# Performance work log

Measured on AMD Instinct MI355X. Metric: run time of the kernel, lower is better.

## Reference

```python
import jax, jax.numpy as jnp
import numpy as np

B, N, E, F, C = 4, 10000, 160000, 128, 128
NUM_ITERATIONS = 3  # num_iterations init arg


def setup_inputs() -> dict:
    key = jax.random.key(0)
    ks = jax.random.split(key, 8)
    objects = jax.random.normal(ks[0], (B, N, F), dtype=jnp.float32)
    connections = jax.random.randint(ks[1], (B, E, 2), 0, N, dtype=jnp.int32)
    # small init scales keep exp() in the attention numerically tame (mirrors
    # glorot/orthogonal-scale weights at init)
    object_state_W = jax.random.normal(ks[2], (F, C), dtype=jnp.float32) * (1.0 / np.sqrt(F))
    state_attention_W = jax.random.normal(ks[3], (C, C), dtype=jnp.float32) * 0.05
    linked_state_attention_W = jax.random.normal(ks[4], (C, C), dtype=jnp.float32) * 0.05
    linked_state_W = jax.random.normal(ks[5], (C, C), dtype=jnp.float32) * (1.0 / np.sqrt(C))
    attention_b = jnp.zeros((C,), dtype=jnp.float32)
    state_b = jnp.zeros((C,), dtype=jnp.float32)
    return {
        "objects": objects,
        "object_state_W": object_state_W,
        "state_attention_W": state_attention_W,
        "linked_state_attention_W": linked_state_attention_W,
        "attention_b": attention_b,
        "linked_state_W": linked_state_W,
        "state_b": state_b,
        "connections": connections,
    }


def reference(objects, object_state_W, state_attention_W, linked_state_attention_W,
              attention_b, linked_state_W, state_b, connections):
    # bidirectional: double edges with both orientations  [B, 2E]
    src = jnp.concatenate([connections[:, :, 0], connections[:, :, 1]], axis=1)
    dst = jnp.concatenate([connections[:, :, 1], connections[:, :, 0]], axis=1)

    # initial states: [B, N, C]
    states = jnp.tanh(jnp.einsum('bnf,fc->bnc', objects, object_state_W) + state_b)

    def step_one(states_b, src_b, dst_b):
        # states_b: [N, C]; src_b/dst_b: [2E]
        states_aW = states_b @ state_attention_W          # [N, C]
        linked_aW = states_b @ linked_state_attention_W   # [N, C]
        # per-edge unnormalized attention  [2E, C]
        attention = jnp.exp(states_aW[src_b] + linked_aW[dst_b] + attention_b)
        # scatter-add normalization; self edge contributes 1 (exp(0))
        attention_norm = jnp.ones_like(states_b).at[src_b].add(attention)  # [N, C]
        self_attention = 1.0 / attention_norm
        attention = attention / attention_norm[src_b]
        # weighted neighbor aggregation
        attented = attention * states_b[dst_b]                              # [2E, C]
        linked_gated = jnp.zeros_like(states_b).at[src_b].add(attented)     # [N, C]
        return jnp.tanh(states_b * self_attention + linked_gated @ linked_state_W + state_b)

    step = jax.vmap(step_one)
    for _ in range(NUM_ITERATIONS):
        states = step(states, src, dst)
    return states
```

## Files before the change

kernel.cpp:

```cpp
#include <hip/hip_runtime.h>
#include <hip/hip_bf16.h>


#define BATCH 4
#define NNODE 10000
#define NEDGE 160000
#define TWOE  (2*NEDGE)
#define MROWS (BATCH*NNODE)
#define NCHUNK 64
#define CHUNKE (NEDGE/NCHUNK)
#define PADN  10240

typedef unsigned short u16;
typedef unsigned int   u32;
typedef __attribute__((ext_vector_type(8))) short bf16x8_t;
typedef __attribute__((ext_vector_type(4))) float f32x4_t;

__device__ __forceinline__ float b2f(u16 h){ return __uint_as_float(((u32)h) << 16); }
__device__ __forceinline__ u16 f2bf(float f){
  u32 u = __float_as_uint(f);
  return (u16)((u + 0x7fffu + ((u >> 16) & 1u)) >> 16);
}
__device__ __forceinline__ float fast_tanh(float x){
  float e = __expf(2.0f * x);
  return fmaf(-2.0f, __builtin_amdgcn_rcpf(e + 1.0f), 1.0f);
}

__global__ void detect_dtype(const u32* __restrict__ objw, int* __restrict__ flag){
  __shared__ int zc, hc;
  if (threadIdx.x == 0){ zc = 0; hc = 0; }
  __syncthreads();
  int z = 0, h = 0;
  for (int i = threadIdx.x; i < 1024; i += 256){
    u32 lo = objw[i] & 0xffffu;
    if (lo == 0) z++;
    if (((lo >> 7) & 0xffu) >= 160u) h++;
  }
  atomicAdd(&zc, z); atomicAdd(&hc, h);
  __syncthreads();
  if (threadIdx.x == 0) *flag = (hc > 0 || zc > 512) ? 1 : 0;
}

__global__ void prep_weights(const void* __restrict__ Wo, const void* __restrict__ Wa,
                             const void* __restrict__ Wla, const void* __restrict__ Wl,
                             const void* __restrict__ ab, const void* __restrict__ sb,
                             const int* __restrict__ flag, u16* __restrict__ Wt,
                             float* __restrict__ biasf){
  int idx = blockIdx.x * 256 + threadIdx.x;
  bool f = (*flag != 0);
  if (idx < 65536){
    int m = idx >> 14, k = (idx >> 7) & 127, c = idx & 127;
    const void* src = (m == 0) ? Wo : (m == 1) ? Wa : (m == 2) ? Wla : Wl;
    u16 h = f ? f2bf(((const float*)src)[k * 128 + c]) : ((const u16*)src)[k * 128 + c];
    Wt[m * 16384 + c * 128 + k] = h;
  } else {
    int t = idx - 65536;
    const void* src = (t < 128) ? sb : ab;
    int i = t & 127;
    biasf[t] = f ? ((const float*)src)[i] : b2f(((const u16*)src)[i]);
  }
}

__device__ __forceinline__ void chunk_of(int blk, int& b, int& c){
  int xcd = blk & 7;
  b = xcd >> 1;
  c = ((blk >> 3) << 1) | (xcd & 1);
}

__global__ void __launch_bounds__(256) csr_hist(const int* __restrict__ conn,
                                                u16* __restrict__ partial){
  int b, c; chunk_of(blockIdx.x, b, c);
  __shared__ u32 hist[NNODE];
  for (int n = threadIdx.x; n < NNODE; n += 256) hist[n] = 0;
  __syncthreads();
  const int2* cp = (const int2*)conn + (size_t)b * NEDGE + c * CHUNKE;
  for (int i = threadIdx.x; i < CHUNKE; i += 256){
    int2 e = cp[i];
    atomicAdd(&hist[e.x], 1);
    atomicAdd(&hist[e.y], 1);
  }
  __syncthreads();
  u16* prow = partial + (size_t)(b * NCHUNK + c) * PADN;
  for (int n = threadIdx.x; n < NNODE; n += 256) prow[n] = (u16)hist[n];
}

__global__ void __launch_bounds__(256) csr_colscan(u16* __restrict__ partial,
    int* __restrict__ row_start, int* __restrict__ bsum){
  int b = blockIdx.x / 40, w = blockIdx.x % 40;
  int n = w * 256 + threadIdx.x;
  u32 run = 0;
  if (n < NNODE){
    #pragma unroll 8
    for (int c = 0; c < NCHUNK; c++){
      size_t idx = (size_t)(b * NCHUNK + c) * PADN + n;
      u32 v = partial[idx];
      partial[idx] = (u16)run;
      run += v;
    }
  }
  __shared__ u32 buf[256];
  buf[threadIdx.x] = run;
  __syncthreads();
  for (int off = 1; off < 256; off <<= 1){
    u32 x = (threadIdx.x >= (unsigned)off) ? buf[threadIdx.x - off] : 0;
    __syncthreads();
    buf[threadIdx.x] += x;
    __syncthreads();
  }
  u32 incl = buf[threadIdx.x];
  if (n < NNODE) row_start[b * (NNODE + 1) + n] = (int)(incl - run);
  if (threadIdx.x == 255) bsum[blockIdx.x] = (int)incl;
}

__global__ void scanB(const int* __restrict__ bsum, int* __restrict__ boff,
                      int* __restrict__ row_start){
  __shared__ int s[160];
  if (threadIdx.x < 160) s[threadIdx.x] = bsum[threadIdx.x];
  __syncthreads();
  if (threadIdx.x < 160){
    int b = threadIdx.x / 40, j = threadIdx.x % 40;
    int off = 0;
    for (int q = b * 40; q < b * 40 + j; q++) off += s[q];
    boff[threadIdx.x] = off;
  }
  if (threadIdx.x < BATCH) row_start[threadIdx.x * (NNODE + 1) + NNODE] = TWOE;
}

__global__ void scanC(int* __restrict__ row_start, const int* __restrict__ boff){
  int b = blockIdx.x / 40, j = blockIdx.x % 40;
  int n = j * 256 + threadIdx.x;
  if (n < NNODE) row_start[b * (NNODE + 1) + n] += boff[blockIdx.x];
}

__global__ void __launch_bounds__(256) csr_fill(const int* __restrict__ conn,
    const u16* __restrict__ partial, const int* __restrict__ row_start,
    int* __restrict__ edge_dst){
  int b, c; chunk_of(blockIdx.x, b, c);
  __shared__ u32 cur[NNODE];
  const u16* prow = partial + (size_t)(b * NCHUNK + c) * PADN;
  const int* rs = row_start + b * (NNODE + 1);
  for (int n = threadIdx.x; n < NNODE; n += 256) cur[n] = (u32)rs[n] + prow[n];
  __syncthreads();
  const int2* cp = (const int2*)conn + (size_t)b * NEDGE + c * CHUNKE;
  int* edb = edge_dst + (size_t)b * TWOE;
  for (int i = threadIdx.x; i < CHUNKE; i += 256){
    int2 e = cp[i];
    u32 p1 = atomicAdd(&cur[e.x], 1); edb[p1] = e.y;
    u32 p2 = atomicAdd(&cur[e.y], 1); edb[p2] = e.x;
  }
}

__device__ __forceinline__ void gemm_tile4(const u16* __restrict__ arow,
    const u16* __restrict__ wt, int lm, int lq, int cofs, f32x4_t acc[4]){
  #pragma unroll
  for (int ks = 0; ks < 4; ks++){
    bf16x8_t a = *(const bf16x8_t*)(arow + ks * 32);
    #pragma unroll
    for (int nb = 0; nb < 4; nb++){
      bf16x8_t bfr = *(const bf16x8_t*)(wt + (cofs + nb * 16 + lm) * 128 + ks * 32 + lq * 8);
      acc[nb] = __builtin_amdgcn_mfma_f32_16x16x32_bf16(a, bfr, acc[nb], 0, 0, 0);
    }
  }
}

__device__ __forceinline__ void gemm_tile4_packed(const u32* __restrict__ Lrow,
    const u16* __restrict__ wt, int lm, int lq, int cofs, f32x4_t acc[4]){
  #pragma unroll
  for (int ks = 0; ks < 4; ks++){
    uint4 wa = *(const uint4*)(Lrow + ks * 32 + lq * 8);
    uint4 wb = *(const uint4*)(Lrow + ks * 32 + lq * 8 + 4);
    bf16x8_t a;
    a[0] = (short)wa.x; a[1] = (short)wa.y; a[2] = (short)wa.z; a[3] = (short)wa.w;
    a[4] = (short)wb.x; a[5] = (short)wb.y; a[6] = (short)wb.z; a[7] = (short)wb.w;
    #pragma unroll
    for (int nb = 0; nb < 4; nb++){
      bf16x8_t bfr = *(const bf16x8_t*)(wt + (cofs + nb * 16 + lm) * 128 + ks * 32 + lq * 8);
      acc[nb] = __builtin_amdgcn_mfma_f32_16x16x32_bf16(a, bfr, acc[nb], 0, 0, 0);
    }
  }
}

__device__ __forceinline__ void phase2_awlaw4(const u16* __restrict__ ldstile,
    const u16* __restrict__ Wt, const float* __restrict__ biasf,
    int lm, int lq, int cofs, int r0, float* __restrict__ awsa,
    u32* __restrict__ ghw){
  const u16* Wta  = Wt + 16384;
  const u16* Wtla = Wt + 32768;
  const u16* ldsrow = ldstile + lm * 136 + lq * 8;
  f32x4_t accA[4], accL[4];
  #pragma unroll
  for (int i = 0; i < 4; i++){ accA[i] = (f32x4_t){0.f,0.f,0.f,0.f}; accL[i] = (f32x4_t){0.f,0.f,0.f,0.f}; }
  #pragma unroll
  for (int ks = 0; ks < 4; ks++){
    bf16x8_t a = *(const bf16x8_t*)(ldsrow + ks * 32);
    #pragma unroll
    for (int nb = 0; nb < 4; nb++){
      bf16x8_t ba = *(const bf16x8_t*)(Wta  + (cofs + nb * 16 + lm) * 128 + ks * 32 + lq * 8);
      bf16x8_t bl = *(const bf16x8_t*)(Wtla + (cofs + nb * 16 + lm) * 128 + ks * 32 + lq * 8);
      accA[nb] = __builtin_amdgcn_mfma_f32_16x16x32_bf16(a, ba, accA[nb], 0, 0, 0);
      accL[nb] = __builtin_amdgcn_mfma_f32_16x16x32_bf16(a, bl, accL[nb], 0, 0, 0);
    }
  }
  #pragma unroll
  for (int nb = 0; nb < 4; nb++){
    int col = cofs + nb * 16 + lm;
    float bb = biasf[128 + col];
    #pragma unroll
    for (int i = 0; i < 4; i++){
      int row = r0 + lq * 4 + i;
      awsa[(size_t)row * 128 + col] = accA[nb][i];
      u16 el = f2bf(__expf(accL[nb][i] + bb));
      u16 s  = ldstile[(lq * 4 + i) * 136 + col];
      ghw[(size_t)row * 64 + (col & 63)] = (u32)el | ((u32)s << 16);
    }
  }
}

__global__ void __launch_bounds__(256) fused_init(const void* __restrict__ obj_raw,
    const int* __restrict__ flag, const u16* __restrict__ Wt,
    const float* __restrict__ biasf, float* __restrict__ awsa,
    u32* __restrict__ gat0, u32* __restrict__ gat1){
  __shared__ u16 lds[2][16 * 136];
  const int lane = threadIdx.x & 63, wave = threadIdx.x >> 6;
  const int t = wave >> 1, ch = wave & 1, cofs = ch * 64;
  const int r0 = blockIdx.x * 32 + t * 16;
  const int lm = lane & 15, lq = lane >> 4;
  f32x4_t acc[4];
  #pragma unroll
  for (int i = 0; i < 4; i++) acc[i] = (f32x4_t){0.f, 0.f, 0.f, 0.f};
  if (*flag){
    const float* arow = (const float*)obj_raw + (size_t)(r0 + lm) * 128 + lq * 8;
    #pragma unroll
    for (int ks = 0; ks < 4; ks++){
      float4 fa = *(const float4*)(arow + ks * 32);
      float4 fb = *(const float4*)(arow + ks * 32 + 4);
      bf16x8_t a;
      a[0] = (short)f2bf(fa.x); a[1] = (short)f2bf(fa.y);
      a[2] = (short)f2bf(fa.z); a[3] = (short)f2bf(fa.w);
      a[4] = (short)f2bf(fb.x); a[5] = (short)f2bf(fb.y);
      a[6] = (short)f2bf(fb.z); a[7] = (short)f2bf(fb.w);
      #pragma unroll
      for (int nb = 0; nb < 4; nb++){
        bf16x8_t bfr = *(const bf16x8_t*)(Wt + (cofs + nb * 16 + lm) * 128 + ks * 32 + lq * 8);
        acc[nb] = __builtin_amdgcn_mfma_f32_16x16x32_bf16(a, bfr, acc[nb], 0, 0, 0);
      }
    }
  } else {
    gemm_tile4((const u16*)obj_raw + (size_t)(r0 + lm) * 128 + lq * 8, Wt, lm, lq, cofs, acc);
  }
  #pragma unroll
  for (int nb = 0; nb < 4; nb++){
    int col = cofs + nb * 16 + lm;
    float bb = biasf[col];
    #pragma unroll
    for (int i = 0; i < 4; i++)
      lds[t][(lq * 4 + i) * 136 + col] = f2bf(fast_tanh(acc[nb][i] + bb));
  }
  __syncthreads();
  phase2_awlaw4(&lds[t][0], Wt, biasf, lm, lq, cofs, r0, awsa, ch ? gat1 : gat0);
}

__global__ void __launch_bounds__(256) fused_mid(const u32* __restrict__ lgsa,
    const u16* __restrict__ Wt, const float* __restrict__ biasf,
    float* __restrict__ awsa, u32* __restrict__ gat0, u32* __restrict__ gat1){
  __shared__ u16 lds[2][16 * 136];
  const int lane = threadIdx.x & 63, wave = threadIdx.x >> 6;
  const int t = wave >> 1, ch = wave & 1, cofs = ch * 64;
  const int r0 = blockIdx.x * 32 + t * 16;
  const int lm = lane & 15, lq = lane >> 4;
  f32x4_t acc[4];
  #pragma unroll
  for (int i = 0; i < 4; i++) acc[i] = (f32x4_t){0.f, 0.f, 0.f, 0.f};
  gemm_tile4_packed(lgsa + (size_t)(r0 + lm) * 128, Wt + 49152, lm, lq, cofs, acc);
  #pragma unroll
  for (int nb = 0; nb < 4; nb++){
    int col = cofs + nb * 16 + lm;
    float bb = biasf[col];
    #pragma unroll
    for (int i = 0; i < 4; i++){
      int row = r0 + lq * 4 + i;
      u32 v = lgsa[(size_t)row * 128 + col];
      u16 hb = (u16)(v >> 16);
      float sa = (float)(*(const _Float16*)&hb);
      lds[t][(lq * 4 + i) * 136 + col] = f2bf(fast_tanh(sa + acc[nb][i] + bb));
    }
  }
  __syncthreads();
  phase2_awlaw4(&lds[t][0], Wt, biasf, lm, lq, cofs, r0, awsa, ch ? gat1 : gat0);
}

__global__ void __launch_bounds__(256) final_out(const u32* __restrict__ lgsa,
    const u16* __restrict__ Wt, const float* __restrict__ biasf,
    const int* __restrict__ flag, void* __restrict__ outp){
  const int lane = threadIdx.x & 63, wave = threadIdx.x >> 6;
  const int t = wave >> 1, ch = wave & 1, cofs = ch * 64;
  const int r0 = blockIdx.x * 32 + t * 16;
  const int lm = lane & 15, lq = lane >> 4;
  bool f32out = (*flag != 0);
  f32x4_t acc[4];
  #pragma unroll
  for (int i = 0; i < 4; i++) acc[i] = (f32x4_t){0.f, 0.f, 0.f, 0.f};
  gemm_tile4_packed(lgsa + (size_t)(r0 + lm) * 128, Wt + 49152, lm, lq, cofs, acc);
  #pragma unroll
  for (int nb = 0; nb < 4; nb++){
    int col = cofs + nb * 16 + lm;
    float bb = biasf[col];
    #pragma unroll
    for (int i = 0; i < 4; i++){
      int row = r0 + lq * 4 + i;
      u32 vv = lgsa[(size_t)row * 128 + col];
      u16 hb = (u16)(vv >> 16);
      float sa = (float)(*(const _Float16*)&hb);
      float v = fast_tanh(sa + acc[nb][i] + bb);
      if (f32out) ((float*)outp)[(size_t)row * 128 + col] = v;
      else        ((u16*)  outp)[(size_t)row * 128 + col] = f2bf(v);
    }
  }
}

__device__ __forceinline__ void acc_e(u32 g, float& s1, float& s2){
  float el = __uint_as_float(g << 16);
  float sv = __uint_as_float(g & 0xffff0000u);
  s1 += el;
  s2 = fmaf(el, sv, s2);
}

__global__ void __launch_bounds__(256) edge_kernel(const float* __restrict__ awsa,
    const u32* __restrict__ gat0, const u32* __restrict__ gat1,
    const int* __restrict__ row_start, const int* __restrict__ edge_dst,
    u32* __restrict__ lgsa){
  int blk = blockIdx.x;
  int xcd = blk & 7;
  int b = xcd >> 1, h = xcd & 1;
  int i = blk >> 3;
  int n = i * 4 + (int)(threadIdx.x >> 6);
  int node = b * NNODE + n;
  int c = threadIdx.x & 63;
  const u32* gh = (h ? gat1 : gat0) + (size_t)b * NNODE * 64;
  int e0 = __builtin_amdgcn_readfirstlane(row_start[b * (NNODE + 1) + n]);
  int e1 = __builtin_amdgcn_readfirstlane(row_start[b * (NNODE + 1) + n + 1]);
  const int* ed = edge_dst + (size_t)b * TWOE;

  float aw = awsa[(size_t)node * 128 + h * 64 + c];
  float ea = __expf(aw);
  float s1 = 0.f, s2 = 0.f, t1 = 0.f, t2 = 0.f;
  int e = e0;
  for (; e + 8 <= e1; e += 8){
    int d0 = ed[e+0], d1 = ed[e+1], d2 = ed[e+2], d3 = ed[e+3];
    int d4 = ed[e+4], d5 = ed[e+5], d6 = ed[e+6], d7 = ed[e+7];
    u32 g0 = gh[(size_t)d0 * 64 + c];
    u32 g1 = gh[(size_t)d1 * 64 + c];
    u32 g2 = gh[(size_t)d2 * 64 + c];
    u32 g3 = gh[(size_t)d3 * 64 + c];
    u32 g4 = gh[(size_t)d4 * 64 + c];
    u32 g5 = gh[(size_t)d5 * 64 + c];
    u32 g6 = gh[(size_t)d6 * 64 + c];
    u32 g7 = gh[(size_t)d7 * 64 + c];
    acc_e(g0, s1, s2); acc_e(g1, t1, t2);
    acc_e(g2, s1, s2); acc_e(g3, t1, t2);
    acc_e(g4, s1, s2); acc_e(g5, t1, t2);
    acc_e(g6, s1, s2); acc_e(g7, t1, t2);
  }
  for (; e < e1; e++){
    u32 gg = gh[(size_t)ed[e] * 64 + c];
    acc_e(gg, s1, s2);
  }
  s1 += t1; s2 += t2;
  float inv = __builtin_amdgcn_rcpf(fmaf(ea, s1, 1.0f));
  float lg = ea * s2 * inv;
  u32 self = gh[(size_t)n * 64 + c];
  float s_self = __uint_as_float(self & 0xffff0000u);
  _Float16 hs = (_Float16)(s_self * inv);
  u32 pk = (u32)f2bf(lg) | ((u32)(*(const u16*)&hs) << 16);
  lgsa[(size_t)node * 128 + h * 64 + c] = pk;
}

extern "C" void kernel_launch(void* const* d_in, const int* in_sizes, int n_in,
                              void* d_out, int out_size, void* d_ws, size_t ws_size,
                              hipStream_t stream){
  (void)in_sizes; (void)n_in; (void)ws_size; (void)out_size;
  const void* objects = d_in[0];
  const void* Wo      = d_in[1];
  const void* Wa      = d_in[2];
  const void* Wla     = d_in[3];
  const void* attn_b  = d_in[4];
  const void* Wl      = d_in[5];
  const void* state_b = d_in[6];
  const int*  conn    = (const int*)d_in[7];

  char* base = (char*)d_ws;
  size_t off = 0;
  auto alloc = [&](size_t bytes) -> char* {
    char* p = base + off;
    off = (off + bytes + 255) & ~(size_t)255;
    return p;
  };
  int*   flag      = (int*)  alloc(256);
  u16*   Wt        = (u16*)  alloc((size_t)4 * 16384 * 2);
  float* biasf     = (float*)alloc(256 * 4);
  float* awsa      = (float*)alloc((size_t)MROWS * 128 * 4);
  u32*   gat0      = (u32*)  alloc((size_t)MROWS * 64 * 4);
  u32*   gat1      = (u32*)  alloc((size_t)MROWS * 64 * 4);
  u32*   lgsa      = (u32*)  alloc((size_t)MROWS * 128 * 4);
  u16*   partial   = (u16*)  alloc((size_t)BATCH * NCHUNK * PADN * 2);
  int*   row_start = (int*)  alloc((size_t)BATCH * (NNODE + 1) * 4);
  int*   edge_dst  = (int*)  alloc((size_t)BATCH * TWOE * 4);
  int*   bsum      = (int*)  alloc(160 * 4);
  int*   boff      = (int*)  alloc(160 * 4);

  detect_dtype<<<1, 256, 0, stream>>>((const u32*)objects, flag);
  prep_weights<<<257, 256, 0, stream>>>(Wo, Wa, Wla, Wl, attn_b, state_b, flag, Wt, biasf);

  csr_hist<<<256, 256, 0, stream>>>(conn, partial);
  csr_colscan<<<160, 256, 0, stream>>>(partial, row_start, bsum);
  scanB<<<1, 256, 0, stream>>>(bsum, boff, row_start);
  scanC<<<160, 256, 0, stream>>>(row_start, boff);
  csr_fill<<<256, 256, 0, stream>>>(conn, partial, row_start, edge_dst);

  fused_init<<<MROWS / 32, 256, 0, stream>>>(objects, flag, Wt, biasf, awsa, gat0, gat1);
  edge_kernel<<<MROWS / 2, 256, 0, stream>>>(awsa, gat0, gat1, row_start, edge_dst, lgsa);
  fused_mid<<<MROWS / 32, 256, 0, stream>>>(lgsa, Wt, biasf, awsa, gat0, gat1);
  edge_kernel<<<MROWS / 2, 256, 0, stream>>>(awsa, gat0, gat1, row_start, edge_dst, lgsa);
  fused_mid<<<MROWS / 32, 256, 0, stream>>>(lgsa, Wt, biasf, awsa, gat0, gat1);
  edge_kernel<<<MROWS / 2, 256, 0, stream>>>(awsa, gat0, gat1, row_start, edge_dst, lgsa);
  final_out<<<MROWS / 32, 256, 0, stream>>>(lgsa, Wt, biasf, flag, d_out);
}
```

Before: 411.5 us.

## Store exp(state attention) as fp16 and remap dense-kernel blocks per XCD batch

The dense fused kernels now compute exp of the state-attention logits themselves and store them as clamped fp16 rather than raw fp32 logits. This halves that buffer's size and removes the exp from the edge kernel. Block indices are also remapped so each XCD pair handles one batch, which matches the edge kernel's XCD mapping and is meant to improve L2 locality for gat/lgsa between stages. It adds fp16 rounding and a clamp at 60000 on the exponentiated values, plus some idle padding blocks and wave-level bounds checks.

New measurement: 405.7 us. About the same (-1.4%).

```diff
diff --git a/kernel.cpp b/kernel.cpp
--- a/kernel.cpp
+++ b/kernel.cpp
@@ -182,7 +182,7 @@
 
 __device__ __forceinline__ void phase2_awlaw4(const u16* __restrict__ ldstile,
     const u16* __restrict__ Wt, const float* __restrict__ biasf,
-    int lm, int lq, int cofs, int r0, float* __restrict__ awsa,
+    int lm, int lq, int cofs, int gr0, _Float16* __restrict__ eah,
     u32* __restrict__ ghw){
   const u16* Wta  = Wt + 16384;
   const u16* Wtla = Wt + 32768;
@@ -207,8 +207,9 @@
     float bb = biasf[128 + col];
     #pragma unroll
     for (int i = 0; i < 4; i++){
-      int row = r0 + lq * 4 + i;
-      awsa[(size_t)row * 128 + col] = accA[nb][i];
+      int row = gr0 + lq * 4 + i;
+      float ea = fminf(__expf(accA[nb][i]), 60000.0f);
+      eah[(size_t)row * 128 + col] = (_Float16)ea;
       u16 el = f2bf(__expf(accL[nb][i] + bb));
       u16 s  = ldstile[(lq * 4 + i) * 136 + col];
       ghw[(size_t)row * 64 + (col & 63)] = (u32)el | ((u32)s << 16);
@@ -216,20 +217,34 @@
   }
 }
 
+__device__ __forceinline__ bool fused_decode(int blk, int wave, int& b, int& r0,
+                                             int& t, int& ch, bool& valid){
+  int xcd = blk & 7;
+  b = xcd >> 1;
+  int sub = ((blk >> 3) << 1) | (xcd & 1);
+  t = wave >> 1; ch = wave & 1;
+  r0 = sub * 32 + t * 16;
+  valid = (sub < 313) && (r0 < NNODE);
+  if (!valid) r0 = 0;
+  return sub < 313;
+}
+
 __global__ void __launch_bounds__(256) fused_init(const void* __restrict__ obj_raw,
     const int* __restrict__ flag, const u16* __restrict__ Wt,
-    const float* __restrict__ biasf, float* __restrict__ awsa,
+    const float* __restrict__ biasf, _Float16* __restrict__ eah,
     u32* __restrict__ gat0, u32* __restrict__ gat1){
   __shared__ u16 lds[2][16 * 136];
   const int lane = threadIdx.x & 63, wave = threadIdx.x >> 6;
-  const int t = wave >> 1, ch = wave & 1, cofs = ch * 64;
-  const int r0 = blockIdx.x * 32 + t * 16;
+  int b, r0, t, ch; bool valid;
+  if (!fused_decode(blockIdx.x, wave, b, r0, t, ch, valid)) return;
+  const int cofs = ch * 64;
   const int lm = lane & 15, lq = lane >> 4;
+  const int gr0 = b * NNODE + r0;
   f32x4_t acc[4];
   #pragma unroll
   for (int i = 0; i < 4; i++) acc[i] = (f32x4_t){0.f, 0.f, 0.f, 0.f};
   if (*flag){
-    const float* arow = (const float*)obj_raw + (size_t)(r0 + lm) * 128 + lq * 8;
+    const float* arow = (const float*)obj_raw + (size_t)(gr0 + lm) * 128 + lq * 8;
     #pragma unroll
     for (int ks = 0; ks < 4; ks++){
       float4 fa = *(const float4*)(arow + ks * 32);
@@ -246,7 +261,7 @@
       }
     }
   } else {
-    gemm_tile4((const u16*)obj_raw + (size_t)(r0 + lm) * 128 + lq * 8, Wt, lm, lq, cofs, acc);
+    gemm_tile4((const u16*)obj_raw + (size_t)(gr0 + lm) * 128 + lq * 8, Wt, lm, lq, cofs, acc);
   }
   #pragma unroll
   for (int nb = 0; nb < 4; nb++){
@@ -257,28 +272,31 @@
       lds[t][(lq * 4 + i) * 136 + col] = f2bf(fast_tanh(acc[nb][i] + bb));
   }
   __syncthreads();
-  phase2_awlaw4(&lds[t][0], Wt, biasf, lm, lq, cofs, r0, awsa, ch ? gat1 : gat0);
+  if (valid)
+    phase2_awlaw4(&lds[t][0], Wt, biasf, lm, lq, cofs, gr0, eah, ch ? gat1 : gat0);
 }
 
 __global__ void __launch_bounds__(256) fused_mid(const u32* __restrict__ lgsa,
     const u16* __restrict__ Wt, const float* __restrict__ biasf,
-    float* __restrict__ awsa, u32* __restrict__ gat0, u32* __restrict__ gat1){
+    _Float16* __restrict__ eah, u32* __restrict__ gat0, u32* __restrict__ gat1){
   __shared__ u16 lds[2][16 * 136];
   const int lane = threadIdx.x & 63, wave = threadIdx.x >> 6;
-  const int t = wave >> 1, ch = wave & 1, cofs = ch * 64;
-  const int r0 = blockIdx.x * 32 + t * 16;
+  int b, r0, t, ch; bool valid;
+  if (!fused_decode(blockIdx.x, wave, b, r0, t, ch, valid)) return;
+  const int cofs = ch * 64;
   const int lm = lane & 15, lq = lane >> 4;
+  const int gr0 = b * NNODE + r0;
   f32x4_t acc[4];
   #pragma unroll
   for (int i = 0; i < 4; i++) acc[i] = (f32x4_t){0.f, 0.f, 0.f, 0.f};
-  gemm_tile4_packed(lgsa + (size_t)(r0 + lm) * 128, Wt + 49152, lm, lq, cofs, acc);
+  gemm_tile4_packed(lgsa + (size_t)(gr0 + lm) * 128, Wt + 49152, lm, lq, cofs, acc);
   #pragma unroll
   for (int nb = 0; nb < 4; nb++){
     int col = cofs + nb * 16 + lm;
     float bb = biasf[col];
     #pragma unroll
     for (int i = 0; i < 4; i++){
-      int row = r0 + lq * 4 + i;
+      int row = gr0 + lq * 4 + i;
       u32 v = lgsa[(size_t)row * 128 + col];
       u16 hb = (u16)(v >> 16);
       float sa = (float)(*(const _Float16*)&hb);
@@ -286,28 +304,32 @@
     }
   }
   __syncthreads();
-  phase2_awlaw4(&lds[t][0], Wt, biasf, lm, lq, cofs, r0, awsa, ch ? gat1 : gat0);
+  if (valid)
+    phase2_awlaw4(&lds[t][0], Wt, biasf, lm, lq, cofs, gr0, eah, ch ? gat1 : gat0);
 }
 
 __global__ void __launch_bounds__(256) final_out(const u32* __restrict__ lgsa,
     const u16* __restrict__ Wt, const float* __restrict__ biasf,
     const int* __restrict__ flag, void* __restrict__ outp){
   const int lane = threadIdx.x & 63, wave = threadIdx.x >> 6;
-  const int t = wave >> 1, ch = wave & 1, cofs = ch * 64;
-  const int r0 = blockIdx.x * 32 + t * 16;
+  int b, r0, t, ch; bool valid;
+  if (!fused_decode(blockIdx.x, wave, b, r0, t, ch, valid)) return;
+  const int cofs = ch * 64;
   const int lm = lane & 15, lq = lane >> 4;
+  const int gr0 = b * NNODE + r0;
   bool f32out = (*flag != 0);
   f32x4_t acc[4];
   #pragma unroll
   for (int i = 0; i < 4; i++) acc[i] = (f32x4_t){0.f, 0.f, 0.f, 0.f};
-  gemm_tile4_packed(lgsa + (size_t)(r0 + lm) * 128, Wt + 49152, lm, lq, cofs, acc);
+  gemm_tile4_packed(lgsa + (size_t)(gr0 + lm) * 128, Wt + 49152, lm, lq, cofs, acc);
+  if (!valid) return;
   #pragma unroll
   for (int nb = 0; nb < 4; nb++){
     int col = cofs + nb * 16 + lm;
     float bb = biasf[col];
     #pragma unroll
     for (int i = 0; i < 4; i++){
-      int row = r0 + lq * 4 + i;
+      int row = gr0 + lq * 4 + i;
       u32 vv = lgsa[(size_t)row * 128 + col];
       u16 hb = (u16)(vv >> 16);
       float sa = (float)(*(const _Float16*)&hb);
@@ -325,7 +347,7 @@
   s2 = fmaf(el, sv, s2);
 }
 
-__global__ void __launch_bounds__(256) edge_kernel(const float* __restrict__ awsa,
+__global__ void __launch_bounds__(256) edge_kernel(const _Float16* __restrict__ eah,
     const u32* __restrict__ gat0, const u32* __restrict__ gat1,
     const int* __restrict__ row_start, const int* __restrict__ edge_dst,
     u32* __restrict__ lgsa){
@@ -341,8 +363,7 @@
   int e1 = __builtin_amdgcn_readfirstlane(row_start[b * (NNODE + 1) + n + 1]);
   const int* ed = edge_dst + (size_t)b * TWOE;
 
-  float aw = awsa[(size_t)node * 128 + h * 64 + c];
-  float ea = __expf(aw);
+  float ea = (float)eah[(size_t)node * 128 + h * 64 + c];
   float s1 = 0.f, s2 = 0.f, t1 = 0.f, t2 = 0.f;
   int e = e0;
   for (; e + 8 <= e1; e += 8){
@@ -395,18 +416,18 @@
     off = (off + bytes + 255) & ~(size_t)255;
     return p;
   };
-  int*   flag      = (int*)  alloc(256);
-  u16*   Wt        = (u16*)  alloc((size_t)4 * 16384 * 2);
-  float* biasf     = (float*)alloc(256 * 4);
-  float* awsa      = (float*)alloc((size_t)MROWS * 128 * 4);
-  u32*   gat0      = (u32*)  alloc((size_t)MROWS * 64 * 4);
-  u32*   gat1      = (u32*)  alloc((size_t)MROWS * 64 * 4);
-  u32*   lgsa      = (u32*)  alloc((size_t)MROWS * 128 * 4);
-  u16*   partial   = (u16*)  alloc((size_t)BATCH * NCHUNK * PADN * 2);
-  int*   row_start = (int*)  alloc((size_t)BATCH * (NNODE + 1) * 4);
-  int*   edge_dst  = (int*)  alloc((size_t)BATCH * TWOE * 4);
-  int*   bsum      = (int*)  alloc(160 * 4);
-  int*   boff      = (int*)  alloc(160 * 4);
+  int*      flag      = (int*)     alloc(256);
+  u16*      Wt        = (u16*)     alloc((size_t)4 * 16384 * 2);
+  float*    biasf     = (float*)   alloc(256 * 4);
+  _Float16* eah       = (_Float16*)alloc((size_t)MROWS * 128 * 2);
+  u32*      gat0      = (u32*)     alloc((size_t)MROWS * 64 * 4);
+  u32*      gat1      = (u32*)     alloc((size_t)MROWS * 64 * 4);
+  u32*      lgsa      = (u32*)     alloc((size_t)MROWS * 128 * 4);
+  u16*      partial   = (u16*)     alloc((size_t)BATCH * NCHUNK * PADN * 2);
+  int*      row_start = (int*)     alloc((size_t)BATCH * (NNODE + 1) * 4);
+  int*      edge_dst  = (int*)     alloc((size_t)BATCH * TWOE * 4);
+  int*      bsum      = (int*)     alloc(160 * 4);
+  int*      boff      = (int*)     alloc(160 * 4);
 
   detect_dtype<<<1, 256, 0, stream>>>((const u32*)objects, flag);
   prep_weights<<<257, 256, 0, stream>>>(Wo, Wa, Wla, Wl, attn_b, state_b, flag, Wt, biasf);
@@ -417,11 +438,12 @@
   scanC<<<160, 256, 0, stream>>>(row_start, boff);
   csr_fill<<<256, 256, 0, stream>>>(conn, partial, row_start, edge_dst);
 
-  fused_init<<<MROWS / 32, 256, 0, stream>>>(objects, flag, Wt, biasf, awsa, gat0, gat1);
-  edge_kernel<<<MROWS / 2, 256, 0, stream>>>(awsa, gat0, gat1, row_start, edge_dst, lgsa);
-  fused_mid<<<MROWS / 32, 256, 0, stream>>>(lgsa, Wt, biasf, awsa, gat0, gat1);
-  edge_kernel<<<MROWS / 2, 256, 0, stream>>>(awsa, gat0, gat1, row_start, edge_dst, lgsa);
-  fused_mid<<<MROWS / 32, 256, 0, stream>>>(lgsa, Wt, biasf, awsa, gat0, gat1);
-  edge_kernel<<<MROWS / 2, 256, 0, stream>>>(awsa, gat0, gat1, row_start, edge_dst, lgsa);
-  final_out<<<MROWS / 32, 256, 0, stream>>>(lgsa, Wt, biasf, flag, d_out);
-}
+  const int FGRID = 157 * 8;
+  fused_init<<<FGRID, 256, 0, stream>>>(objects, flag, Wt, biasf, eah, gat0, gat1);
+  edge_kernel<<<MROWS / 2, 256, 0, stream>>>(eah, gat0, gat1, row_start, edge_dst, lgsa);
+  fused_mid<<<FGRID, 256, 0, stream>>>(lgsa, Wt, biasf, eah, gat0, gat1);
+  edge_kernel<<<MROWS / 2, 256, 0, stream>>>(eah, gat0, gat1, row_start, edge_dst, lgsa);
+  fused_mid<<<FGRID, 256, 0, stream>>>(lgsa, Wt, biasf, eah, gat0, gat1);
+  edge_kernel<<<MROWS / 2, 256, 0, stream>>>(eah, gat0, gat1, row_start, edge_dst, lgsa);
+  final_out<<<FGRID, 256, 0, stream>>>(lgsa, Wt, biasf, flag, d_out);
+}
```
